# Optimization experiments

Measured on AMD Instinct MI355X. Metric: run time of the kernel, lower is better.

The kernel has to match this reference:

```python
import jax, jax.numpy as jnp
import numpy as np

NUM_EMBEDDINGS = 8192
EMBEDDING_DIM = 256
COMMITMENT_COST = 0.25
DECAY = 0.99
EPS = 1e-05


def setup_inputs() -> dict:
    key = jax.random.key(0)
    k1, k2, k3 = jax.random.split(key, 3)
    z = jax.random.normal(k1, (32, 1024, EMBEDDING_DIM), dtype=jnp.float32)
    embedding = jax.random.normal(k2, (NUM_EMBEDDINGS, EMBEDDING_DIM), dtype=jnp.float32)
    ema_cluster_size = jnp.zeros((NUM_EMBEDDINGS,), dtype=jnp.float32)
    ema_w = jax.random.normal(k3, (NUM_EMBEDDINGS, EMBEDDING_DIM), dtype=jnp.float32)
    return {"z": z, "embedding": embedding,
            "ema_cluster_size": ema_cluster_size, "ema_w": ema_w}


def reference(z, embedding, ema_cluster_size, ema_w):
    K, D = embedding.shape
    flat_z = z.reshape(-1, D)                                     # [N, D]

    # squared-distance matrix [N, K]: |z|^2 + |e|^2 - 2 z.e
    distances = (jnp.sum(flat_z * flat_z, axis=1, keepdims=True)
                 + jnp.sum(embedding * embedding, axis=1)
                 - 2.0 * flat_z @ embedding.T)
    indices = jnp.argmin(distances, axis=1)                       # [N] int

    # one-hot @ embedding == row gather
    z_q_flat = embedding[indices]                                 # [N, D]

    # --- training-mode EMA update (one-hot sums == scatter-adds) ---
    counts = jax.ops.segment_sum(jnp.ones_like(indices, dtype=flat_z.dtype),
                                 indices, num_segments=K)         # sum(encodings, 0)
    new_cluster_size = ema_cluster_size * DECAY + (1.0 - DECAY) * counts
    dw = jax.ops.segment_sum(flat_z, indices, num_segments=K)     # encodings.T @ flat_z
    new_ema_w = ema_w * DECAY + (1.0 - DECAY) * dw
    n = jnp.sum(new_cluster_size)
    cluster_size = (new_cluster_size + EPS) / (n + K * EPS) * n
    new_embedding = new_ema_w / cluster_size[:, None]

    # commitment loss uses z_q computed with the OLD embedding (detached)
    loss = COMMITMENT_COST * jnp.mean(
        (jax.lax.stop_gradient(z_q_flat) - flat_z) ** 2)
    # straight-through estimator
    z_q = flat_z + jax.lax.stop_gradient(z_q_flat - flat_z)
    z_q = z_q.reshape(z.shape)
    return z_q, loss, indices, new_embedding, new_cluster_size, new_ema_w
```

## Files before the change

kernel.cpp:

```cpp
#include <hip/hip_runtime.h>
#include <cfloat>

#define K_CODES 8192
#define DIM     256
#define NROWS   32768

#define O_ZQ    0
#define O_LOSS  8388608
#define O_IDX   8388609
#define O_NEMB  8421377
#define O_NCS   10518529
#define O_NEMAW 10526721

#define NCH          2
#define CODES_PER_CH (K_CODES / NCH)
#define NT_TILES     (CODES_PER_CH / 256)
#define KT_PER_NT    24
#define KT_TOTAL     (NT_TILES * KT_PER_NT)
#define LDS_BYTES    131072

typedef __attribute__((ext_vector_type(8))) short short8;
typedef __attribute__((ext_vector_type(4))) float floatx4;

__device__ __forceinline__ unsigned short f2bf_rne(float x) {
    unsigned u = __float_as_uint(x);
    u += 0x7fffu + ((u >> 16) & 1u);
    return (unsigned short)(u >> 16);
}
__device__ __forceinline__ float bf2f(unsigned short h) {
    return __uint_as_float(((unsigned)h) << 16);
}
__device__ __forceinline__ void async16(const void* g, void* l) {
    __builtin_amdgcn_global_load_lds(
        (const __attribute__((address_space(1))) void*)g,
        (__attribute__((address_space(3))) void*)l, 16, 0, 0);
}
__device__ __forceinline__ unsigned ldsaddr(const void* p) {
    return (unsigned)(unsigned long long)
        (const __attribute__((address_space(3))) void*)p;
}
#define DSR(dst, addr, off)                                                     \
    asm volatile("ds_read_b128 %0, %1 offset:" #off : "=v"(dst) : "v"(addr))
#define WAITL(n)                                                                \
    do {                                                                        \
        asm volatile("s_waitcnt lgkmcnt(" #n ")" ::: "memory");                 \
        __builtin_amdgcn_sched_barrier(0);                                      \
    } while (0)

__global__ void k_prep(const float* __restrict__ z, const float* __restrict__ emb,
                       unsigned short* __restrict__ zcat, unsigned short* __restrict__ ecat,
                       float* __restrict__ esq, int* __restrict__ zero16k) {
    const int b = blockIdx.x;
    if (b < 8192) {
        const int i = b * 256 + threadIdx.x;
        const int row = i >> 6;
        const int col = (i & 63) << 2;
        float4 v = ((const float4*)z)[i];
        float nx = -2.0f * v.x, ny = -2.0f * v.y, nz = -2.0f * v.z, nw = -2.0f * v.w;
        ushort4 h, l;
        h.x = f2bf_rne(nx); l.x = f2bf_rne(nx - bf2f(h.x));
        h.y = f2bf_rne(ny); l.y = f2bf_rne(ny - bf2f(h.y));
        h.z = f2bf_rne(nz); l.z = f2bf_rne(nz - bf2f(h.z));
        h.w = f2bf_rne(nw); l.w = f2bf_rne(nw - bf2f(h.w));
        *(ushort4*)&zcat[(size_t)row * 512 + col]       = h;
        *(ushort4*)&zcat[(size_t)row * 512 + 256 + col] = l;
    } else {
        const int gid  = (b - 8192) * 256 + threadIdx.x;
        if (gid < 2 * K_CODES) zero16k[gid] = 0;
        const int code = gid >> 6;
        const int lane = gid & 63;
        const int col  = lane << 2;
        float4 v = ((const float4*)emb)[code * 64 + lane];
        ushort4 h, l;
        h.x = f2bf_rne(v.x); l.x = f2bf_rne(v.x - bf2f(h.x));
        h.y = f2bf_rne(v.y); l.y = f2bf_rne(v.y - bf2f(h.y));
        h.z = f2bf_rne(v.z); l.z = f2bf_rne(v.z - bf2f(h.z));
        h.w = f2bf_rne(v.w); l.w = f2bf_rne(v.w - bf2f(h.w));
        *(ushort4*)&ecat[(size_t)code * 512 + col]       = h;
        *(ushort4*)&ecat[(size_t)code * 512 + 256 + col] = l;
        float s = fmaf(v.x, v.x, fmaf(v.y, v.y, fmaf(v.z, v.z, v.w * v.w)));
#pragma unroll
        for (int off = 32; off > 0; off >>= 1) s += __shfl_down(s, off, 64);
        if (lane == 0) esq[code] = s;
    }
}

__global__ __launch_bounds__(512, 2) void k_argmin_mfma(
        const unsigned short* __restrict__ zcat, const unsigned short* __restrict__ ecat,
        const float* __restrict__ esq,
        float* __restrict__ part_v, int* __restrict__ part_i) {
    extern __shared__ __align__(16) unsigned short s_all[];
    const int t    = threadIdx.x;
    const int w    = t >> 6;
    const int lane = t & 63;
    const int quad = lane >> 4;
    const int m    = lane & 15;
    const int wr   = w >> 2;
    const int wc   = w & 3;
    const int row0   = blockIdx.x * 256;
    const int cbase0 = blockIdx.y * CODES_PER_CH;

    const int prow = t >> 2;
    const int pch  = t & 3;
    const int lc   = pch ^ ((prow >> 1) & 3);
    const unsigned short* aSrc = zcat + (size_t)(row0 + prow) * 512 + lc * 8;
    const unsigned short* bSrc = ecat + (size_t)(cbase0 + prow) * 512 + lc * 8;
    const int dstU = prow * 32 + pch * 8;

    const int xo2 = (quad ^ ((m >> 1) & 3)) << 4;
    const unsigned lb = ldsaddr(s_all);
    const unsigned aRdTB = lb + (unsigned)((wr * 128 + m) * 64 + xo2);
    const unsigned bRdTB = lb + 16384u + (unsigned)((wc * 64 + m) * 64 + xo2);

    float    best_v[32];
    unsigned best_p[8];
#pragma unroll
    for (int r = 0; r < 32; ++r) best_v[r] = FLT_MAX;
#pragma unroll
    for (int i = 0; i < 8; ++i) best_p[i] = 0u;

#pragma unroll
    for (int G = 0; G < 3; ++G) {
        const int k0   = G * 32;
        const int offA = (k0 & 255) | ((k0 & 512) >> 1);
        const int offB = k0 & 511;
        unsigned short* dA = s_all + G * 16384 + dstU;
        async16(aSrc + offA, dA);
        async16(aSrc + 65536 + offA, dA + 4096);
        async16(bSrc + offB, dA + 8192);
        async16(bSrc + 65536 + offB, dA + 12288);
    }
    float es[4];
#pragma unroll
    for (int j = 0; j < 4; ++j) es[j] = esq[cbase0 + wc * 64 + j * 16 + m];

#define CL(iacc, areg)                                                          \
    do {                                                                        \
        acc[iacc][0] = __builtin_amdgcn_mfma_f32_16x16x32_bf16(                 \
            areg, bf[0], acc[iacc][0], 0, 0, 0);                                \
        acc[iacc][1] = __builtin_amdgcn_mfma_f32_16x16x32_bf16(                 \
            areg, bf[1], acc[iacc][1], 0, 0, 0);                                \
        acc[iacc][2] = __builtin_amdgcn_mfma_f32_16x16x32_bf16(                 \
            areg, bf[2], acc[iacc][2], 0, 0, 0);                                \
        acc[iacc][3] = __builtin_amdgcn_mfma_f32_16x16x32_bf16(                 \
            areg, bf[3], acc[iacc][3], 0, 0, 0);                                \
    } while (0)

    for (int nt = 0; nt < NT_TILES; ++nt) {
        floatx4 acc[8][4];
#pragma unroll
        for (int j = 0; j < 4; ++j) {
            const float e = es[j];
#pragma unroll
            for (int i = 0; i < 8; ++i) acc[i][j] = (floatx4){e, e, e, e};
        }

#pragma unroll 1
        for (int kk = 0; kk < KT_PER_NT; ++kk) {
            const int g = nt * KT_PER_NT + kk;
            if (g < KT_TOTAL - 2)
                asm volatile("s_waitcnt vmcnt(8)" ::: "memory");
            else if (g == KT_TOTAL - 2)
                asm volatile("s_waitcnt vmcnt(4)" ::: "memory");
            else
                asm volatile("s_waitcnt vmcnt(0)" ::: "memory");
            __builtin_amdgcn_s_barrier();
            __builtin_amdgcn_sched_barrier(0);

            const int G = g + 3;
            if (G < KT_TOTAL) {
                const int ntS = G / KT_PER_NT;
                const int k0  = (G - ntS * KT_PER_NT) * 32;
                const unsigned short* sA = aSrc + ((k0 & 255) | ((k0 & 512) >> 1));
                const unsigned short* sB = bSrc + (size_t)ntS * 131072 + (k0 & 511);
                unsigned short* dD = s_all + (G & 3) * 16384 + dstU;
                async16(sA, dD);
                async16(sA + 65536, dD + 4096);
                async16(sB, dD + 8192);
                async16(sB + 65536, dD + 12288);
            }
            const unsigned bub   = (unsigned)((g & 3) << 15);
            const unsigned addrA = aRdTB + bub;
            const unsigned addrB = bRdTB + bub;

            short8 af[4], bf[4];
            DSR(bf[0], addrB, 0);    DSR(bf[1], addrB, 1024);
            DSR(bf[2], addrB, 2048); DSR(bf[3], addrB, 3072);
            DSR(af[0], addrA, 0);    DSR(af[1], addrA, 1024);
            DSR(af[2], addrA, 2048); DSR(af[3], addrA, 3072);
            __builtin_amdgcn_s_setprio(1);
            WAITL(3); CL(0, af[0]);
            WAITL(2); CL(1, af[1]);
            WAITL(1); CL(2, af[2]);
            DSR(af[0], addrA, 4096);
            DSR(af[1], addrA, 5120);
            DSR(af[2], addrA, 6144);
            WAITL(3); CL(3, af[3]);
            DSR(af[3], addrA, 7168);
            WAITL(3); CL(4, af[0]);
            WAITL(2); CL(5, af[1]);
            WAITL(1); CL(6, af[2]);
            WAITL(0); CL(7, af[3]);
            __builtin_amdgcn_s_setprio(0);
        }
#pragma unroll
        for (int j = 0; j < 4; ++j) {
            const unsigned cand = (unsigned)(nt * 4 + j);
#pragma unroll
            for (int i = 0; i < 8; ++i)
#pragma unroll
                for (int reg = 0; reg < 4; ++reg) {
                    const float s = acc[i][j][reg];
                    const int r = i * 4 + reg;
                    if (s < best_v[r]) {
                        best_v[r] = s;
                        best_p[i] = (best_p[i] & ~(255u << (reg * 8))) | (cand << (reg * 8));
                    }
                }
        }
        if (nt + 1 < NT_TILES) {
#pragma unroll
            for (int j = 0; j < 4; ++j)
                es[j] = esq[cbase0 + (nt + 1) * 256 + wc * 64 + j * 16 + m];
        }
    }
#undef CL
    __syncthreads();
    float* redv = (float*)s_all;
    int*   redi = (int*)(s_all + 2048);
#pragma unroll
    for (int i = 0; i < 8; ++i)
#pragma unroll
        for (int reg = 0; reg < 4; ++reg) {
            const int r = i * 4 + reg;
            const unsigned b = (best_p[i] >> (reg * 8)) & 255u;
            float v  = best_v[r];
            int   bi = cbase0 + (int)(b >> 2) * 256 + wc * 64 + (int)(b & 3) * 16 + m;
#pragma unroll
            for (int off = 1; off < 16; off <<= 1) {
                const float ov = __shfl_xor(v, off, 64);
                const int   oi = __shfl_xor(bi, off, 64);
                if (ov < v || (ov == v && oi < bi)) { v = ov; bi = oi; }
            }
            if (m == 0) {
                const int rl = wr * 128 + i * 16 + quad * 4 + reg;
                redv[rl * 4 + wc] = v;
                redi[rl * 4 + wc] = bi;
            }
        }
    __syncthreads();
    if (t < 256) {
        float v = redv[t * 4]; int bi = redi[t * 4];
#pragma unroll
        for (int c = 1; c < 4; ++c) {
            const float v2 = redv[t * 4 + c];
            const int   i2 = redi[t * 4 + c];
            if (v2 < v || (v2 == v && i2 < bi)) { v = v2; bi = i2; }
        }
        const size_t o = (size_t)blockIdx.y * NROWS + blockIdx.x * 256 + t;
        part_v[o] = v;
        part_i[o] = bi;
    }
}

__global__ void k_reduce_part(const float* __restrict__ pv, const int* __restrict__ pi,
                              int* __restrict__ idx_i, float* __restrict__ idx_f,
                              int* __restrict__ counts) {
    const int r = blockIdx.x * blockDim.x + threadIdx.x;
    float v = pv[r]; int bi = pi[r];
#pragma unroll
    for (int c = 1; c < NCH; ++c) {
        const float v2 = pv[(size_t)c * NROWS + r];
        const int   i2 = pi[(size_t)c * NROWS + r];
        if (v2 < v || (v2 == v && i2 < bi)) { v = v2; bi = i2; }
    }
    idx_i[r] = bi;
    idx_f[r] = (float)bi;
    atomicAdd(&counts[bi], 1);
}

__global__ void k_scan_ncs(const int* __restrict__ counts, const float* __restrict__ ema_cs,
                           int* __restrict__ offsets, float* __restrict__ ncs_out,
                           float* __restrict__ ntot) {
    __shared__ int   wsum[16];
    __shared__ float red[16];
    const int t = threadIdx.x;
    const int lane = t & 63, w = t >> 6;
    int c[8]; int s = 0; float fs = 0.0f;
#pragma unroll
    for (int u = 0; u < 8; ++u) {
        c[u] = counts[t * 8 + u]; s += c[u];
        const float v = fmaf(0.99f, ema_cs[t * 8 + u], 0.01f * (float)c[u]);
        ncs_out[t * 8 + u] = v;
        fs += v;
    }
    int inc = s;
#pragma unroll
    for (int off = 1; off < 64; off <<= 1) {
        const int n = __shfl_up(inc, off, 64);
        if (lane >= off) inc += n;
    }
#pragma unroll
    for (int off = 32; off > 0; off >>= 1) fs += __shfl_down(fs, off, 64);
    if (lane == 63) wsum[w] = inc;
    if (lane == 0)  red[w]  = fs;
    __syncthreads();
    if (t < 16) {
        int v = wsum[t];
#pragma unroll
        for (int off = 1; off < 16; off <<= 1) {
            const int n = __shfl_up(v, off, 64);
            if (t >= off) v += n;
        }
        wsum[t] = v;
        float fv = red[t];
#pragma unroll
        for (int off = 8; off > 0; off >>= 1) fv += __shfl_down(fv, off, 16);
        if (t == 0) *ntot = fv;
    }
    __syncthreads();
    int base = (w > 0 ? wsum[w - 1] : 0) + (inc - s);
#pragma unroll
    for (int u = 0; u < 8; ++u) { offsets[t * 8 + u] = base; base += c[u]; }
}

__global__ void k_zq(const float* __restrict__ z, const float* __restrict__ emb,
                     const int* __restrict__ idx_i, const int* __restrict__ offsets,
                     int* __restrict__ cursor, int* __restrict__ buckets,
                     float* __restrict__ zq, float* __restrict__ losspart) {
    __shared__ float lred[4];
    const int t = threadIdx.x;
    const int wr = t >> 6, lane = t & 63;
    const int row = blockIdx.x * 4 + wr;
    const int code = idx_i[row];
    float4 zv = ((const float4*)z)[row * 64 + lane];
    float4 ev = ((const float4*)emb)[(size_t)code * 64 + lane];
    float4 o = make_float4(zv.x + (ev.x - zv.x), zv.y + (ev.y - zv.y),
                           zv.z + (ev.z - zv.z), zv.w + (ev.w - zv.w));
    ((float4*)zq)[row * 64 + lane] = o;
    float dx = ev.x - zv.x, dy = ev.y - zv.y, dz = ev.z - zv.z, dw = ev.w - zv.w;
    float s = fmaf(dx, dx, fmaf(dy, dy, fmaf(dz, dz, dw * dw)));
#pragma unroll
    for (int off = 32; off > 0; off >>= 1) s += __shfl_down(s, off, 64);
    if (lane == 0) {
        lred[wr] = s;
        const int pos = atomicAdd(&cursor[code], 1);
        buckets[offsets[code] + pos] = row;
    }
    __syncthreads();
    if (t == 0) losspart[blockIdx.x] = (lred[0] + lred[1]) + (lred[2] + lred[3]);
}

__global__ void k_dw_nemb(const float* __restrict__ z, const float* __restrict__ ema_w,
                          const int* __restrict__ counts, const int* __restrict__ offsets,
                          const int* __restrict__ buckets, const float* __restrict__ ncs,
                          const float* __restrict__ ntot_p, const float* __restrict__ losspart,
                          float* __restrict__ nemaw, float* __restrict__ nemb,
                          float* __restrict__ loss_out) {
    __shared__ float lred[4];
    if (blockIdx.x == K_CODES) {
        const int t = threadIdx.x;
        float s = 0.0f;
        for (int i = t; i < 8192; i += 256) s += losspart[i];
#pragma unroll
        for (int off = 32; off > 0; off >>= 1) s += __shfl_down(s, off, 64);
        if ((t & 63) == 0) lred[t >> 6] = s;
        __syncthreads();
        if (t == 0)
            *loss_out = 0.25f * ((lred[0] + lred[1]) + (lred[2] + lred[3])) / 8388608.0f;
        return;
    }
    const int code = blockIdx.x;
    const int d    = threadIdx.x;
    const int cnt  = counts[code];
    const int off  = offsets[code];
    float acc = 0.0f;
    for (int it = 0; it < cnt; ++it)
        acc += z[(size_t)buckets[off + it] * DIM + d];
    const float wv = fmaf(0.99f, ema_w[(size_t)code * DIM + d], 0.01f * acc);
    nemaw[(size_t)code * DIM + d] = wv;
    const float n  = *ntot_p;
    const float cs = (ncs[code] + 1e-5f) * (n / (n + (float)K_CODES * 1e-5f));
    nemb[(size_t)code * DIM + d] = wv / cs;
}

#define BM   64
#define BN   128
#define LSTR 36

__global__ void k_esq_zero_fb(const float* __restrict__ emb, float* __restrict__ esq,
                              float* __restrict__ zbuf) {
    const int gid  = blockIdx.x * blockDim.x + threadIdx.x;
    if (gid < K_CODES + 2) zbuf[gid] = 0.0f;
    const int code = gid >> 6;
    const int lane = gid & 63;
    float4 v = ((const float4*)emb)[code * 64 + lane];
    float s = fmaf(v.x, v.x, fmaf(v.y, v.y, fmaf(v.z, v.z, v.w * v.w)));
#pragma unroll
    for (int off = 32; off > 0; off >>= 1) s += __shfl_down(s, off, 64);
    if (lane == 0) esq[code] = s;
}

__global__ void k_init_nemaw_fb(const float* __restrict__ ema_w, float* __restrict__ out) {
    const int i = blockIdx.x * blockDim.x + threadIdx.x;
    float4 v = ((const float4*)ema_w)[i];
    ((float4*)out)[i] = make_float4(0.99f * v.x, 0.99f * v.y, 0.99f * v.z, 0.99f * v.w);
}

__global__ __launch_bounds__(256, 2) void k_argmin_fb(
        const float* __restrict__ z, const float* __restrict__ emb,
        const float* __restrict__ esq, int* __restrict__ idx_i, float* __restrict__ idx_f) {
    __shared__ float z_s[BM * LSTR];
    __shared__ float e_s[BN * LSTR];
    const int t = threadIdx.x, tx = t & 15, ty = t >> 4;
    const int row0 = blockIdx.x * BM;
    float best[4]; int bidx[4];
#pragma unroll
    for (int r = 0; r < 4; ++r) { best[r] = FLT_MAX; bidx[r] = 0; }
    for (int k0 = 0; k0 < K_CODES; k0 += BN) {
        float acc[4][8];
#pragma unroll
        for (int r = 0; r < 4; ++r)
#pragma unroll
            for (int c = 0; c < 8; ++c) acc[r][c] = 0.0f;
        for (int d0 = 0; d0 < DIM; d0 += 32) {
            __syncthreads();
#pragma unroll
            for (int i = 0; i < 2; ++i) {
                int f = i * 256 + t, r = f >> 3, c4 = (f & 7) << 2;
                *(float4*)&z_s[r * LSTR + c4] =
                    *(const float4*)(z + (size_t)(row0 + r) * DIM + d0 + c4);
            }
#pragma unroll
            for (int i = 0; i < 4; ++i) {
                int f = i * 256 + t, c = f >> 3, c4 = (f & 7) << 2;
                *(float4*)&e_s[c * LSTR + c4] =
                    *(const float4*)(emb + (size_t)(k0 + c) * DIM + d0 + c4);
            }
            __syncthreads();
#pragma unroll
            for (int dd = 0; dd < 32; dd += 4) {
                float4 a[4], b[8];
#pragma unroll
                for (int j = 0; j < 4; ++j)
                    a[j] = *(const float4*)&z_s[(ty * 4 + j) * LSTR + dd];
#pragma unroll
                for (int j = 0; j < 8; ++j)
                    b[j] = *(const float4*)&e_s[(tx + 16 * j) * LSTR + dd];
#pragma unroll
                for (int r = 0; r < 4; ++r)
#pragma unroll
                    for (int c = 0; c < 8; ++c) {
                        acc[r][c] = fmaf(a[r].x, b[c].x, acc[r][c]);
                        acc[r][c] = fmaf(a[r].y, b[c].y, acc[r][c]);
                        acc[r][c] = fmaf(a[r].z, b[c].z, acc[r][c]);
                        acc[r][c] = fmaf(a[r].w, b[c].w, acc[r][c]);
                    }
            }
        }
#pragma unroll
        for (int c = 0; c < 8; ++c) {
            const int code = k0 + tx + 16 * c;
            const float es = esq[code];
#pragma unroll
            for (int r = 0; r < 4; ++r) {
                float s = fmaf(-2.0f, acc[r][c], es);
                if (s < best[r] || (s == best[r] && code < bidx[r])) {
                    best[r] = s; bidx[r] = code;
                }
            }
        }
    }
    __syncthreads();
    float* rv = e_s; int* ri = (int*)z_s;
#pragma unroll
    for (int r = 0; r < 4; ++r) {
        rv[(ty * 4 + r) * 16 + tx] = best[r];
        ri[(ty * 4 + r) * 16 + tx] = bidx[r];
    }
    __syncthreads();
    if (t < 64) {
        float mv = rv[t * 16]; int mi = ri[t * 16];
#pragma unroll
        for (int i = 1; i < 16; ++i) {
            float v = rv[t * 16 + i]; int vi = ri[t * 16 + i];
            if (v < mv || (v == mv && vi < mi)) { mv = v; mi = vi; }
        }
        idx_i[row0 + t] = mi;
        idx_f[row0 + t] = (float)mi;
    }
}

__global__ void k_gather_fb(const float* __restrict__ z, const float* __restrict__ emb,
                            const int* __restrict__ idx_i, float* __restrict__ zq,
                            float* __restrict__ nemaw, float* __restrict__ counts,
                            float* __restrict__ loss) {
    const int gid  = blockIdx.x * blockDim.x + threadIdx.x;
    const int row  = gid >> 6;
    const int lane = gid & 63;
    const int code = idx_i[row];
    float4 zv = ((const float4*)z)[row * 64 + lane];
    float4 ev = ((const float4*)emb)[(size_t)code * 64 + lane];
    float4 o = make_float4(zv.x + (ev.x - zv.x), zv.y + (ev.y - zv.y),
                           zv.z + (ev.z - zv.z), zv.w + (ev.w - zv.w));
    ((float4*)zq)[row * 64 + lane] = o;
    float dx = ev.x - zv.x, dy = ev.y - zv.y, dz = ev.z - zv.z, dw = ev.w - zv.w;
    float s = fmaf(dx, dx, fmaf(dy, dy, fmaf(dz, dz, dw * dw)));
#pragma unroll
    for (int off = 32; off > 0; off >>= 1) s += __shfl_down(s, off, 64);
    if (lane == 0) { atomicAdd(loss, s); atomicAdd(&counts[code], 1.0f); }
    float* base = nemaw + (size_t)code * DIM + lane * 4;
    atomicAdd(base + 0, 0.01f * zv.x);
    atomicAdd(base + 1, 0.01f * zv.y);
    atomicAdd(base + 2, 0.01f * zv.z);
    atomicAdd(base + 3, 0.01f * zv.w);
}

__global__ void k_ncs_fb(const float* __restrict__ ema_cs, const float* __restrict__ counts,
                         float* __restrict__ ncs_out, float* __restrict__ ntot,
                         const float* __restrict__ loss_in, float* __restrict__ loss_out) {
    __shared__ float red[16];
    const int t = threadIdx.x;
    float s = 0.0f;
    for (int i = t; i < K_CODES; i += 1024) {
        float v = fmaf(0.99f, ema_cs[i], 0.01f * counts[i]);
        ncs_out[i] = v; s += v;
    }
#pragma unroll
    for (int off = 32; off > 0; off >>= 1) s += __shfl_down(s, off, 64);
    if ((t & 63) == 0) red[t >> 6] = s;
    __syncthreads();
    if (t < 16) {
        float v = red[t];
#pragma unroll
        for (int off = 8; off > 0; off >>= 1) v += __shfl_down(v, off, 16);
        if (t == 0) { *ntot = v; *loss_out = 0.25f * (*loss_in) / 8388608.0f; }
    }
}

__global__ void k_nemb_fb(const float* __restrict__ nemaw, const float* __restrict__ ncs,
                          const float* __restrict__ ntot_p, float* __restrict__ nemb) {
    const int i4 = blockIdx.x * blockDim.x + threadIdx.x;
    const int k  = i4 >> 6;
    const float n   = *ntot_p;
    const float inv = n / (n + (float)K_CODES * 1e-5f);
    const float cs  = (ncs[k] + 1e-5f) * inv;
    float4 wv = ((const float4*)nemaw)[i4];
    ((float4*)nemb)[i4] = make_float4(wv.x / cs, wv.y / cs, wv.z / cs, wv.w / cs);
}

extern "C" void kernel_launch(void* const* d_in, const int* in_sizes, int n_in,
                              void* d_out, int out_size, void* d_ws, size_t ws_size,
                              hipStream_t stream) {
    const float* z      = (const float*)d_in[0];
    const float* emb    = (const float*)d_in[1];
    const float* ema_cs = (const float*)d_in[2];
    const float* ema_w  = (const float*)d_in[3];
    float* out = (float*)d_out;
    char* wsb = (char*)d_ws;

    unsigned short* zcat    = (unsigned short*)wsb;
    unsigned short* ecat    = (unsigned short*)(wsb + 33554432);
    float*          part_v  = (float*)(wsb + 41943040);
    int*            part_i  = (int*)  (wsb + 42467328);
    float*          esq     = (float*)(wsb + 42991616);
    int*            ws_idx  = (int*)  (wsb + 43024384);
    int*            counts  = (int*)  (wsb + 43155456);
    int*            cursor  = (int*)  (wsb + 43188224);
    int*            offsets = (int*)  (wsb + 43220992);
    int*            buckets = (int*)  (wsb + 43253760);
    float*          lpart   = (float*)(wsb + 43384832);
    float*          ws_loss = (float*)(wsb + 43417600);
    float*          ws_ntot = ws_loss + 1;

    if (ws_size >= (size_t)43417616) {
        static bool lds_attr_set = false;
        if (!lds_attr_set) {
            (void)hipFuncSetAttribute((const void*)k_argmin_mfma,
                                      hipFuncAttributeMaxDynamicSharedMemorySize,
                                      LDS_BYTES);
            lds_attr_set = true;
        }
        k_prep       <<<10240, 256, 0, stream>>>(z, emb, zcat, ecat, esq, counts);
        k_argmin_mfma<<<dim3(NROWS / 256, NCH), 512, LDS_BYTES, stream>>>(
            zcat, ecat, esq, part_v, part_i);
        k_reduce_part<<<NROWS / 256, 256, 0, stream>>>(part_v, part_i, ws_idx,
                                                       out + O_IDX, counts);
        k_scan_ncs   <<<1, 1024, 0, stream>>>(counts, ema_cs, offsets,
                                              out + O_NCS, ws_ntot);
        k_zq         <<<NROWS / 4, 256, 0, stream>>>(z, emb, ws_idx, offsets, cursor,
                                                     buckets, out + O_ZQ, lpart);
        k_dw_nemb    <<<K_CODES + 1, 256, 0, stream>>>(z, ema_w, counts, offsets, buckets,
                                                       out + O_NCS, ws_ntot, lpart,
                                                       out + O_NEMAW, out + O_NEMB,
                                                       out + O_LOSS);
    } else {
        int*   f_idx    = (int*)wsb;
        float* f_counts = (float*)(wsb + 131072);
        float* f_loss   = f_counts + K_CODES;
        float* f_ntot   = f_loss + 1;
        float* f_esq    = (float*)(wsb + 163856);
        k_esq_zero_fb  <<<2048, 256, 0, stream>>>(emb, f_esq, f_counts);
        k_init_nemaw_fb<<<2048, 256, 0, stream>>>(ema_w, out + O_NEMAW);
        k_argmin_fb    <<<NROWS / BM, 256, 0, stream>>>(z, emb, f_esq, f_idx, out + O_IDX);
        k_gather_fb    <<<NROWS / 4, 256, 0, stream>>>(z, emb, f_idx, out + O_ZQ,
                                                       out + O_NEMAW, f_counts, f_loss);
        k_ncs_fb       <<<1, 1024, 0, stream>>>(ema_cs, f_counts, out + O_NCS, f_ntot,
                                                f_loss, out + O_LOSS);
        k_nemb_fb      <<<2048, 256, 0, stream>>>(out + O_NEMAW, out + O_NCS, f_ntot,
                                                  out + O_NEMB);
    }
}
```

Baseline: 639.5 us.

## Enlarge per-wave MFMA tile to 128x128 with 4-wave blocks

The argmin GEMM kernel moves from 8 waves per block, each owning a 128x64 output tile, to 4 waves per block, each owning a 128x128 tile. Each thread now issues 8 async loads per stage instead of 4, and the reduction is adjusted to a 2-way merge. The aim is higher arithmetic intensity per LDS read, with fewer B-fragment loads per MFMA. In exchange the accumulators double to 256 floats per thread, which raises register pressure and lowers occupancy, so there are fewer waves to hide latency. The esq prefetch for the next tile is also moved ahead of the argmin update.

```diff
diff --git a/kernel.cpp b/kernel.cpp
--- a/kernel.cpp
+++ b/kernel.cpp
@@ -85,7 +85,7 @@
     }
 }
 
-__global__ __launch_bounds__(512, 2) void k_argmin_mfma(
+__global__ __launch_bounds__(256, 1) void k_argmin_mfma(
         const unsigned short* __restrict__ zcat, const unsigned short* __restrict__ ecat,
         const float* __restrict__ esq,
         float* __restrict__ part_v, int* __restrict__ part_i) {
@@ -95,8 +95,8 @@
     const int lane = t & 63;
     const int quad = lane >> 4;
     const int m    = lane & 15;
-    const int wr   = w >> 2;
-    const int wc   = w & 3;
+    const int wr   = w >> 1;
+    const int wc   = w & 1;
     const int row0   = blockIdx.x * 256;
     const int cbase0 = blockIdx.y * CODES_PER_CH;
 
@@ -110,7 +110,7 @@
     const int xo2 = (quad ^ ((m >> 1) & 3)) << 4;
     const unsigned lb = ldsaddr(s_all);
     const unsigned aRdTB = lb + (unsigned)((wr * 128 + m) * 64 + xo2);
-    const unsigned bRdTB = lb + 16384u + (unsigned)((wc * 64 + m) * 64 + xo2);
+    const unsigned bRdTB = lb + 16384u + (unsigned)((wc * 128 + m) * 64 + xo2);
 
     float    best_v[32];
     unsigned best_p[8];
@@ -124,32 +124,29 @@
         const int k0   = G * 32;
         const int offA = (k0 & 255) | ((k0 & 512) >> 1);
         const int offB = k0 & 511;
-        unsigned short* dA = s_all + G * 16384 + dstU;
-        async16(aSrc + offA, dA);
-        async16(aSrc + 65536 + offA, dA + 4096);
-        async16(bSrc + offB, dA + 8192);
-        async16(bSrc + 65536 + offB, dA + 12288);
-    }
-    float es[4];
-#pragma unroll
-    for (int j = 0; j < 4; ++j) es[j] = esq[cbase0 + wc * 64 + j * 16 + m];
+        unsigned short* dD = s_all + G * 16384 + dstU;
+#pragma unroll
+        for (int p = 0; p < 4; ++p) {
+            async16(aSrc + p * 32768 + offA, dD + p * 2048);
+            async16(bSrc + p * 32768 + offB, dD + 8192 + p * 2048);
+        }
+    }
+    float es[8];
+#pragma unroll
+    for (int j = 0; j < 8; ++j) es[j] = esq[cbase0 + wc * 128 + j * 16 + m];
 
 #define CL(iacc, areg)                                                          \
     do {                                                                        \
-        acc[iacc][0] = __builtin_amdgcn_mfma_f32_16x16x32_bf16(                 \
-            areg, bf[0], acc[iacc][0], 0, 0, 0);                                \
-        acc[iacc][1] = __builtin_amdgcn_mfma_f32_16x16x32_bf16(                 \
-            areg, bf[1], acc[iacc][1], 0, 0, 0);                                \
-        acc[iacc][2] = __builtin_amdgcn_mfma_f32_16x16x32_bf16(                 \
-            areg, bf[2], acc[iacc][2], 0, 0, 0);                                \
-        acc[iacc][3] = __builtin_amdgcn_mfma_f32_16x16x32_bf16(                 \
-            areg, bf[3], acc[iacc][3], 0, 0, 0);                                \
+        _Pragma("unroll")                                                       \
+        for (int j_ = 0; j_ < 8; ++j_)                                          \
+            acc[iacc][j_] = __builtin_amdgcn_mfma_f32_16x16x32_bf16(            \
+                areg, bf[j_], acc[iacc][j_], 0, 0, 0);                          \
     } while (0)
 
     for (int nt = 0; nt < NT_TILES; ++nt) {
-        floatx4 acc[8][4];
-#pragma unroll
-        for (int j = 0; j < 4; ++j) {
+        floatx4 acc[8][8];
+#pragma unroll
+        for (int j = 0; j < 8; ++j) {
             const float e = es[j];
 #pragma unroll
             for (int i = 0; i < 8; ++i) acc[i][j] = (floatx4){e, e, e, e};
@@ -159,9 +156,9 @@
         for (int kk = 0; kk < KT_PER_NT; ++kk) {
             const int g = nt * KT_PER_NT + kk;
             if (g < KT_TOTAL - 2)
+                asm volatile("s_waitcnt vmcnt(16)" ::: "memory");
+            else if (g == KT_TOTAL - 2)
                 asm volatile("s_waitcnt vmcnt(8)" ::: "memory");
-            else if (g == KT_TOTAL - 2)
-                asm volatile("s_waitcnt vmcnt(4)" ::: "memory");
             else
                 asm volatile("s_waitcnt vmcnt(0)" ::: "memory");
             __builtin_amdgcn_s_barrier();
@@ -174,38 +171,47 @@
                 const unsigned short* sA = aSrc + ((k0 & 255) | ((k0 & 512) >> 1));
                 const unsigned short* sB = bSrc + (size_t)ntS * 131072 + (k0 & 511);
                 unsigned short* dD = s_all + (G & 3) * 16384 + dstU;
-                async16(sA, dD);
-                async16(sA + 65536, dD + 4096);
-                async16(sB, dD + 8192);
-                async16(sB + 65536, dD + 12288);
+#pragma unroll
+                for (int p = 0; p < 4; ++p) {
+                    async16(sA + p * 32768, dD + p * 2048);
+                    async16(sB + p * 32768, dD + 8192 + p * 2048);
+                }
             }
             const unsigned bub   = (unsigned)((g & 3) << 15);
             const unsigned addrA = aRdTB + bub;
             const unsigned addrB = bRdTB + bub;
 
-            short8 af[4], bf[4];
+            short8 af[8], bf[8];
             DSR(bf[0], addrB, 0);    DSR(bf[1], addrB, 1024);
             DSR(bf[2], addrB, 2048); DSR(bf[3], addrB, 3072);
+            DSR(bf[4], addrB, 4096); DSR(bf[5], addrB, 5120);
+            DSR(bf[6], addrB, 6144); DSR(bf[7], addrB, 7168);
             DSR(af[0], addrA, 0);    DSR(af[1], addrA, 1024);
-            DSR(af[2], addrA, 2048); DSR(af[3], addrA, 3072);
             __builtin_amdgcn_s_setprio(1);
-            WAITL(3); CL(0, af[0]);
-            WAITL(2); CL(1, af[1]);
+            WAITL(1); CL(0, af[0]);
+            DSR(af[2], addrA, 2048);
+            WAITL(1); CL(1, af[1]);
+            DSR(af[3], addrA, 3072);
             WAITL(1); CL(2, af[2]);
-            DSR(af[0], addrA, 4096);
-            DSR(af[1], addrA, 5120);
-            DSR(af[2], addrA, 6144);
-            WAITL(3); CL(3, af[3]);
-            DSR(af[3], addrA, 7168);
-            WAITL(3); CL(4, af[0]);
-            WAITL(2); CL(5, af[1]);
-            WAITL(1); CL(6, af[2]);
-            WAITL(0); CL(7, af[3]);
+            DSR(af[4], addrA, 4096);
+            WAITL(1); CL(3, af[3]);
+            DSR(af[5], addrA, 5120);
+            WAITL(1); CL(4, af[4]);
+            DSR(af[6], addrA, 6144);
+            WAITL(1); CL(5, af[5]);
+            DSR(af[7], addrA, 7168);
+            WAITL(1); CL(6, af[6]);
+            WAITL(0); CL(7, af[7]);
             __builtin_amdgcn_s_setprio(0);
         }
-#pragma unroll
-        for (int j = 0; j < 4; ++j) {
-            const unsigned cand = (unsigned)(nt * 4 + j);
+        if (nt + 1 < NT_TILES) {
+#pragma unroll
+            for (int j = 0; j < 8; ++j)
+                es[j] = esq[cbase0 + (nt + 1) * 256 + wc * 128 + j * 16 + m];
+        }
+#pragma unroll
+        for (int j = 0; j < 8; ++j) {
+            const unsigned cand = (unsigned)(nt * 8 + j);
 #pragma unroll
             for (int i = 0; i < 8; ++i)
 #pragma unroll
@@ -218,16 +224,11 @@
                     }
                 }
         }
-        if (nt + 1 < NT_TILES) {
-#pragma unroll
-            for (int j = 0; j < 4; ++j)
-                es[j] = esq[cbase0 + (nt + 1) * 256 + wc * 64 + j * 16 + m];
-        }
     }
 #undef CL
     __syncthreads();
     float* redv = (float*)s_all;
-    int*   redi = (int*)(s_all + 2048);
+    int*   redi = (int*)(s_all + 1024);
 #pragma unroll
     for (int i = 0; i < 8; ++i)
 #pragma unroll
@@ -235,7 +236,7 @@
             const int r = i * 4 + reg;
             const unsigned b = (best_p[i] >> (reg * 8)) & 255u;
             float v  = best_v[r];
-            int   bi = cbase0 + (int)(b >> 2) * 256 + wc * 64 + (int)(b & 3) * 16 + m;
+            int   bi = cbase0 + (int)(b >> 3) * 256 + wc * 128 + (int)(b & 7) * 16 + m;
 #pragma unroll
             for (int off = 1; off < 16; off <<= 1) {
                 const float ov = __shfl_xor(v, off, 64);
@@ -244,22 +245,18 @@
             }
             if (m == 0) {
                 const int rl = wr * 128 + i * 16 + quad * 4 + reg;
-                redv[rl * 4 + wc] = v;
-                redi[rl * 4 + wc] = bi;
+                redv[rl * 2 + wc] = v;
+                redi[rl * 2 + wc] = bi;
             }
         }
     __syncthreads();
-    if (t < 256) {
-        float v = redv[t * 4]; int bi = redi[t * 4];
-#pragma unroll
-        for (int c = 1; c < 4; ++c) {
-            const float v2 = redv[t * 4 + c];
-            const int   i2 = redi[t * 4 + c];
-            if (v2 < v || (v2 == v && i2 < bi)) { v = v2; bi = i2; }
-        }
+    {
+        const float v0 = redv[t * 2], v1 = redv[t * 2 + 1];
+        const int   i0 = redi[t * 2], i1 = redi[t * 2 + 1];
+        const bool  b1 = (v1 < v0) || (v1 == v0 && i1 < i0);
         const size_t o = (size_t)blockIdx.y * NROWS + blockIdx.x * 256 + t;
-        part_v[o] = v;
-        part_i[o] = bi;
+        part_v[o] = b1 ? v1 : v0;
+        part_i[o] = b1 ? i1 : i0;
     }
 }
 
@@ -582,7 +579,7 @@
             lds_attr_set = true;
         }
         k_prep       <<<10240, 256, 0, stream>>>(z, emb, zcat, ecat, esq, counts);
-        k_argmin_mfma<<<dim3(NROWS / 256, NCH), 512, LDS_BYTES, stream>>>(
+        k_argmin_mfma<<<dim3(NROWS / 256, NCH), 256, LDS_BYTES, stream>>>(
             zcat, ecat, esq, part_v, part_i);
         k_reduce_part<<<NROWS / 256, 256, 0, stream>>>(part_v, part_i, ws_idx,
                                                        out + O_IDX, counts);
```

Measured after the change: 1.110 ms. 73.5% more time.
